# Kernel tuning notes

Hardware: AMD Instinct MI355X
Metric: run time of the kernel (lower is better)

The kernel has to match this reference:

```python
import jax, jax.numpy as jnp
import numpy as np

TEMPERATURE = 8.0  # sqrt(d_k), d_k = 64

def setup_inputs() -> dict:
    key = jax.random.key(0)
    k1, k2, k3, k4 = jax.random.split(key, 4)
    B, H, S, D = 2, 16, 2048, 64
    q = jax.random.normal(k1, (B, H, S, D), dtype=jnp.float32)
    k = jax.random.normal(k2, (B, H, S, D), dtype=jnp.float32)
    v = jax.random.normal(k3, (B, H, S, D), dtype=jnp.float32)
    # dwm: distance-weight matrix broadcast over heads
    dwm = jax.random.uniform(k4, (B, 1, S, S), dtype=jnp.float32)
    sigma = jnp.ones((1,), dtype=jnp.float32)
    return {"q": q, "k": k, "v": v, "dwm": dwm, "sigma": sigma}

def reference(q, k, v, dwm, sigma):
    # scores: [B,H,S,S]
    attn = jnp.einsum("bhsd,bhtd->bhst", q / TEMPERATURE, k)
    g = jnp.exp(dwm / (sigma ** 2))  # broadcasts [B,1,S,S] -> [B,H,S,S]
    attn = jnp.abs(attn * g)
    attn = jax.nn.softmax(attn, axis=-1)  # dropout is identity in eval
    output = jnp.einsum("bhst,bhtd->bhsd", attn, v)
    return (output, attn)
```

## Files before the change

### kernel.cpp

```cpp
#include <hip/hip_runtime.h>
#include <hip/hip_fp16.h>

#define NB 2
#define NH 16
#define NS 2048
#define ND 64
#define BM 64
#define BN 64
#define NT (NS / BN)
#define TILE_BYTES 24576
#define KV_BYTES ((size_t)NB * NH * NT * TILE_BYTES)

#define SW(r) ((((r) & 7) ^ (((r) & 8) >> 2)) << 4)

typedef _Float16 half8 __attribute__((ext_vector_type(8)));
typedef _Float16 half4 __attribute__((ext_vector_type(4)));
typedef float f32x4 __attribute__((ext_vector_type(4)));

#define GLDS16(gp, lp) __builtin_amdgcn_global_load_lds(                      \
    (const __attribute__((address_space(1))) void*)(gp),                      \
    (__attribute__((address_space(3))) void*)(lp), 16, 0, 0)

__global__ __launch_bounds__(256)
void prep_kv(const float* __restrict__ kg, const float* __restrict__ vg,
             char* __restrict__ ws)
{
    __shared__ _Float16 T[64][72];
    const int tile = blockIdx.x, bh = blockIdx.y, tid = threadIdx.x;
    const float* kp = kg + ((size_t)bh * NS + (size_t)tile * BN) * ND;
    const float* vp = vg + ((size_t)bh * NS + (size_t)tile * BN) * ND;
    char* img = ws + ((size_t)(bh * NT + tile)) * TILE_BYTES;

    #pragma unroll
    for (int i = 0; i < 2; ++i) {
        const int c = tid + i * 256;
        const int r = c >> 3, s = c & 7;
        const float* src = kp + r * ND + s * 8;
        float4 f0 = *(const float4*)src;
        float4 f1 = *(const float4*)(src + 4);
        float fv[8] = {f0.x, f0.y, f0.z, f0.w, f1.x, f1.y, f1.z, f1.w};
        half8 h, l;
        #pragma unroll
        for (int j = 0; j < 8; ++j) {
            _Float16 hh = (_Float16)fv[j];
            h[j] = hh; l[j] = (_Float16)(fv[j] - (float)hh);
        }
        const int off = r * 128 + ((s << 4) ^ SW(r));
        *(half8*)(img + off) = h;
        *(half8*)(img + 8192 + off) = l;
    }
    #pragma unroll
    for (int i = 0; i < 2; ++i) {
        const int c = tid + i * 256;
        const int t = c >> 3, ds = (c & 7) * 8;
        const float* src = vp + t * ND + ds;
        float4 f0 = *(const float4*)src;
        float4 f1 = *(const float4*)(src + 4);
        float fv[8] = {f0.x, f0.y, f0.z, f0.w, f1.x, f1.y, f1.z, f1.w};
        #pragma unroll
        for (int j = 0; j < 8; ++j) T[t][ds + j] = (_Float16)fv[j];
    }
    __syncthreads();
    #pragma unroll
    for (int i = 0; i < 2; ++i) {
        const int c = tid + i * 256;
        const int d = c >> 3, s = c & 7;
        half8 h;
        #pragma unroll
        for (int j = 0; j < 8; ++j) h[j] = T[s * 8 + j][d];
        *(half8*)(img + 16384 + d * 128 + ((s << 4) ^ SW(d))) = h;
    }
}

__global__ __launch_bounds__(256, 5)
void attn_fused(const float* __restrict__ qg, const char* __restrict__ kvws,
                const float* __restrict__ dwm, const float* __restrict__ sig,
                float* __restrict__ out0, float* __restrict__ attn)
{
    __shared__ char lds[32768];
    char* const Khi = lds;
    char* const Klo = lds + 8192;
    char* const Vs  = lds + 16384;
    char* const Ps  = lds + 24576;

    const int tid  = threadIdx.x;
    const int wave = tid >> 6;
    const int lane = tid & 63;
    const int quad = lane >> 4;
    const int lc   = lane & 15;

    const int mtile = blockIdx.x;
    const int bh    = blockIdx.y;
    const int b     = bh >> 4;

    const float sv = sig[0];
    const float inv_s2 = 1.0f / (sv * sv);

    const float* qp  = qg  + (size_t)bh * NS * ND + (size_t)mtile * BM * ND;
    const char*  kvb = kvws + (size_t)bh * NT * TILE_BYTES;
    const float* dp  = dwm + (size_t)b  * NS * NS + (size_t)mtile * BM * NS;
    float* op = out0 + (size_t)bh * NS * ND + (size_t)mtile * BM * ND;
    float* ap = attn + (size_t)bh * NS * NS + (size_t)mtile * BM * NS;

    half8 aqh0, aql0, aqh1, aql1;
    {
        const float* qr = qp + (size_t)(wave * 16 + lc) * ND + quad * 8;
        float4 f0 = *(const float4*)qr;
        float4 f1 = *(const float4*)(qr + 4);
        float4 f2 = *(const float4*)(qr + 32);
        float4 f3 = *(const float4*)(qr + 36);
        float v0[8] = {f0.x, f0.y, f0.z, f0.w, f1.x, f1.y, f1.z, f1.w};
        float v1[8] = {f2.x, f2.y, f2.z, f2.w, f3.x, f3.y, f3.z, f3.w};
        #pragma unroll
        for (int j = 0; j < 8; j++) {
            float x = v0[j] * 0.125f;
            _Float16 h = (_Float16)x;
            aqh0[j] = h; aql0[j] = (_Float16)(x - (float)h);
            x = v1[j] * 0.125f;
            h = (_Float16)x;
            aqh1[j] = h; aql1[j] = (_Float16)(x - (float)h);
        }
    }

    float lsum[4] = {0.f, 0.f, 0.f, 0.f};

    for (int t = 0; t < NT; ++t) {
        const char* img = kvb + (size_t)t * TILE_BYTES;
        __syncthreads();
        GLDS16(img +         tid * 16, Khi +        tid * 16);
        GLDS16(img +  4096 + tid * 16, Khi + 4096 + tid * 16);
        GLDS16(img +  8192 + tid * 16, Klo +        tid * 16);
        GLDS16(img + 12288 + tid * 16, Klo + 4096 + tid * 16);
        __syncthreads();
        #pragma unroll
        for (int n = 0; n < 4; ++n) {
            const int rowK = n * 16 + lc;
            const int sw = SW(rowK);
            const char* kb = Khi + rowK * 128;
            const char* lb = Klo + rowK * 128;
            const half8 kh0 = *(const half8*)(kb + ((quad * 16) ^ sw));
            const half8 kh1 = *(const half8*)(kb + ((64 + quad * 16) ^ sw));
            const half8 kl0 = *(const half8*)(lb + ((quad * 16) ^ sw));
            const half8 kl1 = *(const half8*)(lb + ((64 + quad * 16) ^ sw));
            f32x4 c = {0.f, 0.f, 0.f, 0.f};
            c = __builtin_amdgcn_mfma_f32_16x16x32_f16(aqh0, kh0, c, 0, 0, 0);
            c = __builtin_amdgcn_mfma_f32_16x16x32_f16(aqh1, kh1, c, 0, 0, 0);
            c = __builtin_amdgcn_mfma_f32_16x16x32_f16(aql0, kh0, c, 0, 0, 0);
            c = __builtin_amdgcn_mfma_f32_16x16x32_f16(aql1, kh1, c, 0, 0, 0);
            c = __builtin_amdgcn_mfma_f32_16x16x32_f16(aqh0, kl0, c, 0, 0, 0);
            c = __builtin_amdgcn_mfma_f32_16x16x32_f16(aqh1, kl1, c, 0, 0, 0);
            #pragma unroll
            for (int r2 = 0; r2 < 4; ++r2) {
                const int lrow = wave * 16 + quad * 4 + r2;
                const int col  = t * BN + n * 16 + lc;
                const float g = __expf(dp[(size_t)lrow * NS + col] * inv_s2);
                lsum[r2] += __expf(fabsf(c[r2]) * g);
            }
        }
    }

    #pragma unroll
    for (int r2 = 0; r2 < 4; ++r2) {
        float s = lsum[r2];
        s += __shfl_xor(s, 1, 64);
        s += __shfl_xor(s, 2, 64);
        s += __shfl_xor(s, 4, 64);
        s += __shfl_xor(s, 8, 64);
        lsum[r2] = 1.0f / s;
    }

    f32x4 o[4];
    #pragma unroll
    for (int i = 0; i < 4; i++) o[i] = (f32x4){0.f, 0.f, 0.f, 0.f};

    for (int t = 0; t < NT; ++t) {
        const char* img = kvb + (size_t)t * TILE_BYTES;
        __syncthreads();
        GLDS16(img +         tid * 16, Khi +        tid * 16);
        GLDS16(img +  4096 + tid * 16, Khi + 4096 + tid * 16);
        GLDS16(img +  8192 + tid * 16, Klo +        tid * 16);
        GLDS16(img + 12288 + tid * 16, Klo + 4096 + tid * 16);
        GLDS16(img + 16384 + tid * 16, Vs  +        tid * 16);
        GLDS16(img + 20480 + tid * 16, Vs  + 4096 + tid * 16);
        __syncthreads();
        #pragma unroll
        for (int n = 0; n < 4; ++n) {
            const int rowK = n * 16 + lc;
            const int sw = SW(rowK);
            const char* kb = Khi + rowK * 128;
            const char* lb = Klo + rowK * 128;
            const half8 kh0 = *(const half8*)(kb + ((quad * 16) ^ sw));
            const half8 kh1 = *(const half8*)(kb + ((64 + quad * 16) ^ sw));
            const half8 kl0 = *(const half8*)(lb + ((quad * 16) ^ sw));
            const half8 kl1 = *(const half8*)(lb + ((64 + quad * 16) ^ sw));
            f32x4 c = {0.f, 0.f, 0.f, 0.f};
            c = __builtin_amdgcn_mfma_f32_16x16x32_f16(aqh0, kh0, c, 0, 0, 0);
            c = __builtin_amdgcn_mfma_f32_16x16x32_f16(aqh1, kh1, c, 0, 0, 0);
            c = __builtin_amdgcn_mfma_f32_16x16x32_f16(aql0, kh0, c, 0, 0, 0);
            c = __builtin_amdgcn_mfma_f32_16x16x32_f16(aql1, kh1, c, 0, 0, 0);
            c = __builtin_amdgcn_mfma_f32_16x16x32_f16(aqh0, kl0, c, 0, 0, 0);
            c = __builtin_amdgcn_mfma_f32_16x16x32_f16(aqh1, kl1, c, 0, 0, 0);
            #pragma unroll
            for (int r2 = 0; r2 < 4; ++r2) {
                const int lrow = wave * 16 + quad * 4 + r2;
                const int col  = t * BN + n * 16 + lc;
                const float g = __expf(dp[(size_t)lrow * NS + col] * inv_s2);
                const float p = __expf(fabsf(c[r2]) * g) * lsum[r2];
                *(_Float16*)(Ps + lrow * 128 +
                             (((n * 16 + lc) * 2) ^ SW(lrow))) = (_Float16)p;
            }
        }
        const int rowP = wave * 16 + lc;
        const int swp = SW(rowP);
        const half8 pa0 = *(const half8*)(Ps + rowP * 128 + ((quad * 16) ^ swp));
        const half8 pa1 = *(const half8*)(Ps + rowP * 128 + ((64 + quad * 16) ^ swp));

        {
            const int cl = lane & 15, rh = lane >> 4;
            #pragma unroll
            for (int g2 = 0; g2 < 4; ++g2) {
                const int row = wave * 16 + g2 * 4 + rh;
                const half4 ph = *(const half4*)(Ps + row * 128 +
                                                 ((cl * 8) ^ SW(row)));
                f32x4 s = {(float)ph[0], (float)ph[1], (float)ph[2], (float)ph[3]};
                __builtin_nontemporal_store(
                    s, (f32x4*)(ap + (size_t)row * NS + t * BN + cl * 4));
            }
        }

        #pragma unroll
        for (int n2 = 0; n2 < 4; ++n2) {
            const int dv = n2 * 16 + lc;
            const int swv = SW(dv);
            const char* vb = Vs + dv * 128;
            const half8 bv0 = *(const half8*)(vb + ((quad * 16) ^ swv));
            const half8 bv1 = *(const half8*)(vb + ((64 + quad * 16) ^ swv));
            o[n2] = __builtin_amdgcn_mfma_f32_16x16x32_f16(pa0, bv0, o[n2], 0, 0, 0);
            o[n2] = __builtin_amdgcn_mfma_f32_16x16x32_f16(pa1, bv1, o[n2], 0, 0, 0);
        }
    }

    #pragma unroll
    for (int n2 = 0; n2 < 4; ++n2) {
        #pragma unroll
        for (int r2 = 0; r2 < 4; ++r2) {
            const int lrow = wave * 16 + quad * 4 + r2;
            __builtin_nontemporal_store(o[n2][r2],
                                        &op[(size_t)lrow * ND + n2 * 16 + lc]);
        }
    }
}

#define KP 72
#define VP 72
#define PP 72

__global__ __launch_bounds__(256, 4)
void attn_fused_legacy(const float* __restrict__ qg, const float* __restrict__ kgl,
                       const float* __restrict__ vgl, const float* __restrict__ dwm,
                       const float* __restrict__ sig, float* __restrict__ out0,
                       float* __restrict__ attn)
{
    __shared__ _Float16 Khi[BN * KP];
    __shared__ _Float16 Klo[BN * KP];
    __shared__ _Float16 Vsl[ND * VP];
    __shared__ _Float16 Psl[BM * PP];

    const int tid  = threadIdx.x;
    const int wave = tid >> 6;
    const int lane = tid & 63;
    const int quad = lane >> 4;
    const int lc   = lane & 15;

    const int mtile = blockIdx.x;
    const int bh    = blockIdx.y;
    const int b     = bh >> 4;

    const float sv = sig[0];
    const float inv_s2 = 1.0f / (sv * sv);

    const float* qp = qg  + (size_t)bh * NS * ND + (size_t)mtile * BM * ND;
    const float* kp = kgl + (size_t)bh * NS * ND;
    const float* vp = vgl + (size_t)bh * NS * ND;
    const float* dp = dwm + (size_t)b  * NS * NS + (size_t)mtile * BM * NS;
    float* op = out0 + (size_t)bh * NS * ND + (size_t)mtile * BM * ND;
    float* ap = attn + (size_t)bh * NS * NS + (size_t)mtile * BM * NS;

    half8 aqh0, aql0, aqh1, aql1;
    {
        const float* qr = qp + (size_t)(wave * 16 + lc) * ND + quad * 8;
        float4 f0 = *(const float4*)qr;
        float4 f1 = *(const float4*)(qr + 4);
        float4 f2 = *(const float4*)(qr + 32);
        float4 f3 = *(const float4*)(qr + 36);
        float v0[8] = {f0.x, f0.y, f0.z, f0.w, f1.x, f1.y, f1.z, f1.w};
        float v1[8] = {f2.x, f2.y, f2.z, f2.w, f3.x, f3.y, f3.z, f3.w};
        #pragma unroll
        for (int j = 0; j < 8; j++) {
            float x = v0[j] * 0.125f;
            _Float16 h = (_Float16)x;
            aqh0[j] = h; aql0[j] = (_Float16)(x - (float)h);
            x = v1[j] * 0.125f;
            h = (_Float16)x;
            aqh1[j] = h; aql1[j] = (_Float16)(x - (float)h);
        }
    }

    auto stageK = [&](int t0) {
        const int r  = tid >> 2;
        const int ds = (tid & 3) * 16;
        const float* s = kp + (size_t)(t0 + r) * ND + ds;
        float4 f0 = *(const float4*)s;
        float4 f1 = *(const float4*)(s + 4);
        float4 f2 = *(const float4*)(s + 8);
        float4 f3 = *(const float4*)(s + 12);
        float fv[16] = {f0.x, f0.y, f0.z, f0.w, f1.x, f1.y, f1.z, f1.w,
                        f2.x, f2.y, f2.z, f2.w, f3.x, f3.y, f3.z, f3.w};
        half8 h0, h1, l0, l1;
        #pragma unroll
        for (int i = 0; i < 8; i++) {
            _Float16 h = (_Float16)fv[i];
            h0[i] = h; l0[i] = (_Float16)(fv[i] - (float)h);
            h = (_Float16)fv[8 + i];
            h1[i] = h; l1[i] = (_Float16)(fv[8 + i] - (float)h);
        }
        *(half8*)&Khi[r * KP + ds]     = h0;
        *(half8*)&Khi[r * KP + ds + 8] = h1;
        *(half8*)&Klo[r * KP + ds]     = l0;
        *(half8*)&Klo[r * KP + ds + 8] = l1;
    };

    auto stageV = [&](int t0) {
        const int tp = tid >> 3;
        const int ds = (tid & 7) * 8;
        const float4* sa = (const float4*)(vp + (size_t)(t0 + 2 * tp) * ND + ds);
        const float4* sb = (const float4*)(vp + (size_t)(t0 + 2 * tp + 1) * ND + ds);
        float4 a0 = sa[0], a1 = sa[1];
        float4 b0 = sb[0], b1 = sb[1];
        float av[8] = {a0.x, a0.y, a0.z, a0.w, a1.x, a1.y, a1.z, a1.w};
        float bv[8] = {b0.x, b0.y, b0.z, b0.w, b1.x, b1.y, b1.z, b1.w};
        unsigned int* Vdw = (unsigned int*)Vsl;
        #pragma unroll
        for (int i = 0; i < 8; i++) {
            const int d  = ds + i;
            const int dw = d * (VP / 2) + (tp ^ (((d >> 3) & 7) << 2));
            union { _Float16 h[2]; unsigned int u; } pk;
            pk.h[0] = (_Float16)av[i];
            pk.h[1] = (_Float16)bv[i];
            Vdw[dw] = pk.u;
        }
    };

    float lsum[4] = {0.f, 0.f, 0.f, 0.f};

    for (int t0 = 0; t0 < NS; t0 += BN) {
        __syncthreads();
        stageK(t0);
        __syncthreads();
        #pragma unroll
        for (int n = 0; n < 4; n++) {
            const half8 kh0 = *(const half8*)&Khi[(n * 16 + lc) * KP + quad * 8];
            const half8 kh1 = *(const half8*)&Khi[(n * 16 + lc) * KP + quad * 8 + 32];
            const half8 kl0 = *(const half8*)&Klo[(n * 16 + lc) * KP + quad * 8];
            const half8 kl1 = *(const half8*)&Klo[(n * 16 + lc) * KP + quad * 8 + 32];
            f32x4 c = {0.f, 0.f, 0.f, 0.f};
            c = __builtin_amdgcn_mfma_f32_16x16x32_f16(aqh0, kh0, c, 0, 0, 0);
            c = __builtin_amdgcn_mfma_f32_16x16x32_f16(aqh1, kh1, c, 0, 0, 0);
            c = __builtin_amdgcn_mfma_f32_16x16x32_f16(aql0, kh0, c, 0, 0, 0);
            c = __builtin_amdgcn_mfma_f32_16x16x32_f16(aql1, kh1, c, 0, 0, 0);
            c = __builtin_amdgcn_mfma_f32_16x16x32_f16(aqh0, kl0, c, 0, 0, 0);
            c = __builtin_amdgcn_mfma_f32_16x16x32_f16(aqh1, kl1, c, 0, 0, 0);
            #pragma unroll
            for (int r2 = 0; r2 < 4; r2++) {
                const int lrow = wave * 16 + quad * 4 + r2;
                const int col  = t0 + n * 16 + lc;
                const float g = __expf(dp[(size_t)lrow * NS + col] * inv_s2);
                const float z = fabsf(c[r2] * g);
                lsum[r2] += __expf(z);
            }
        }
    }

    #pragma unroll
    for (int r2 = 0; r2 < 4; r2++) {
        float s = lsum[r2];
        s += __shfl_xor(s, 1, 64);
        s += __shfl_xor(s, 2, 64);
        s += __shfl_xor(s, 4, 64);
        s += __shfl_xor(s, 8, 64);
        lsum[r2] = 1.0f / s;
    }

    f32x4 o[4];
    #pragma unroll
    for (int i = 0; i < 4; i++) o[i] = (f32x4){0.f, 0.f, 0.f, 0.f};

    for (int t0 = 0; t0 < NS; t0 += BN) {
        __syncthreads();
        stageK(t0);
        stageV(t0);
        __syncthreads();
        #pragma unroll
        for (int n = 0; n < 4; n++) {
            const half8 kh0 = *(const half8*)&Khi[(n * 16 + lc) * KP + quad * 8];
            const half8 kh1 = *(const half8*)&Khi[(n * 16 + lc) * KP + quad * 8 + 32];
            const half8 kl0 = *(const half8*)&Klo[(n * 16 + lc) * KP + quad * 8];
            const half8 kl1 = *(const half8*)&Klo[(n * 16 + lc) * KP + quad * 8 + 32];
            f32x4 c = {0.f, 0.f, 0.f, 0.f};
            c = __builtin_amdgcn_mfma_f32_16x16x32_f16(aqh0, kh0, c, 0, 0, 0);
            c = __builtin_amdgcn_mfma_f32_16x16x32_f16(aqh1, kh1, c, 0, 0, 0);
            c = __builtin_amdgcn_mfma_f32_16x16x32_f16(aql0, kh0, c, 0, 0, 0);
            c = __builtin_amdgcn_mfma_f32_16x16x32_f16(aql1, kh1, c, 0, 0, 0);
            c = __builtin_amdgcn_mfma_f32_16x16x32_f16(aqh0, kl0, c, 0, 0, 0);
            c = __builtin_amdgcn_mfma_f32_16x16x32_f16(aqh1, kl1, c, 0, 0, 0);
            #pragma unroll
            for (int r2 = 0; r2 < 4; r2++) {
                const int lrow = wave * 16 + quad * 4 + r2;
                const int col  = t0 + n * 16 + lc;
                const float g = __expf(dp[(size_t)lrow * NS + col] * inv_s2);
                const float z = fabsf(c[r2] * g);
                const float p = __expf(z) * lsum[r2];
                Psl[(size_t)lrow * PP + n * 16 + lc] = (_Float16)p;
            }
        }
        const half8 pa0 = *(const half8*)&Psl[(wave * 16 + lc) * PP + quad * 8];
        const half8 pa1 = *(const half8*)&Psl[(wave * 16 + lc) * PP + quad * 8 + 32];

        {
            float* arow = ap + (size_t)(wave * 16 + lc) * NS + t0 + quad * 8;
            f32x4 s0 = {(float)pa0[0], (float)pa0[1], (float)pa0[2], (float)pa0[3]};
            f32x4 s1 = {(float)pa0[4], (float)pa0[5], (float)pa0[6], (float)pa0[7]};
            f32x4 s2 = {(float)pa1[0], (float)pa1[1], (float)pa1[2], (float)pa1[3]};
            f32x4 s3 = {(float)pa1[4], (float)pa1[5], (float)pa1[6], (float)pa1[7]};
            __builtin_nontemporal_store(s0, (f32x4*)arow);
            __builtin_nontemporal_store(s1, (f32x4*)(arow + 4));
            __builtin_nontemporal_store(s2, (f32x4*)(arow + 32));
            __builtin_nontemporal_store(s3, (f32x4*)(arow + 36));
        }

        #pragma unroll
        for (int n2 = 0; n2 < 4; n2++) {
            const int dv  = n2 * 16 + lc;
            const int fd  = ((dv >> 3) & 7) << 2;
            const int dwb = dv * (VP / 2);
            const half8 bv0 = *(const half8*)((const char*)Vsl +
                               (size_t)((dwb + ((quad * 4) ^ fd)) * 4));
            const half8 bv1 = *(const half8*)((const char*)Vsl +
                               (size_t)((dwb + ((16 + quad * 4) ^ fd)) * 4));
            o[n2] = __builtin_amdgcn_mfma_f32_16x16x32_f16(pa0, bv0, o[n2], 0, 0, 0);
            o[n2] = __builtin_amdgcn_mfma_f32_16x16x32_f16(pa1, bv1, o[n2], 0, 0, 0);
        }
    }

    #pragma unroll
    for (int n2 = 0; n2 < 4; n2++) {
        #pragma unroll
        for (int r2 = 0; r2 < 4; r2++) {
            const int lrow = wave * 16 + quad * 4 + r2;
            __builtin_nontemporal_store(o[n2][r2],
                                        &op[(size_t)lrow * ND + n2 * 16 + lc]);
        }
    }
}

extern "C" void kernel_launch(void* const* d_in, const int* in_sizes, int n_in,
                              void* d_out, int out_size, void* d_ws, size_t ws_size,
                              hipStream_t stream) {
    (void)in_sizes; (void)n_in; (void)out_size;
    const float* q   = (const float*)d_in[0];
    const float* k   = (const float*)d_in[1];
    const float* v   = (const float*)d_in[2];
    const float* dwm = (const float*)d_in[3];
    const float* sig = (const float*)d_in[4];
    float* out0 = (float*)d_out;
    float* attn = out0 + (size_t)NB * NH * NS * ND;

    if (d_ws != nullptr && ws_size >= KV_BYTES) {
        char* ws = (char*)d_ws;
        prep_kv<<<dim3(NT, NB * NH), dim3(256), 0, stream>>>(k, v, ws);
        attn_fused<<<dim3(NS / BM, NB * NH), dim3(256), 0, stream>>>(
            q, ws, dwm, sig, out0, attn);
    } else {
        dim3 grid(NS / BM, NB * NH);
        attn_fused_legacy<<<grid, dim3(256), 0, stream>>>(
            q, k, v, dwm, sig, out0, attn);
    }
}
```

Baseline: 864.9 us.

## Double-buffer K tiles in LDS to overlap global loads with compute

Adds a second K hi/lo tile buffer in shared memory and prefetches the next tile with global_load_lds while the current tile is used, in both the row-sum pass and the output pass. Explicit vmcnt waits and barriers replace the paired __syncthreads around each load. The goal is to hide load latency behind MFMA and exp work. In exchange LDS grows from 32 KB to 48 KB and launch bounds drop from 5 to 3 blocks per CU, so occupancy falls. The second pass relies on vmcnt(4) ordering to wait for V while the prefetch stays in flight, which is delicate.

```diff
diff --git a/kernel.cpp b/kernel.cpp
--- a/kernel.cpp
+++ b/kernel.cpp
@@ -72,16 +72,14 @@
     }
 }
 
-__global__ __launch_bounds__(256, 5)
+__global__ __launch_bounds__(256, 3)
 void attn_fused(const float* __restrict__ qg, const char* __restrict__ kvws,
                 const float* __restrict__ dwm, const float* __restrict__ sig,
                 float* __restrict__ out0, float* __restrict__ attn)
 {
-    __shared__ char lds[32768];
-    char* const Khi = lds;
-    char* const Klo = lds + 8192;
-    char* const Vs  = lds + 16384;
-    char* const Ps  = lds + 24576;
+    __shared__ char lds[49152];
+    char* const Vs = lds + 32768;
+    char* const Ps = lds + 40960;
 
     const int tid  = threadIdx.x;
     const int wave = tid >> 6;
@@ -124,24 +122,33 @@
 
     float lsum[4] = {0.f, 0.f, 0.f, 0.f};
 
+    {
+        #pragma unroll
+        for (int j = 0; j < 4; ++j)
+            GLDS16(kvb + j * 4096 + tid * 16, lds + j * 4096 + tid * 16);
+        asm volatile("s_waitcnt vmcnt(0)" ::: "memory");
+        __builtin_amdgcn_s_barrier();
+    }
+
     for (int t = 0; t < NT; ++t) {
-        const char* img = kvb + (size_t)t * TILE_BYTES;
-        __syncthreads();
-        GLDS16(img +         tid * 16, Khi +        tid * 16);
-        GLDS16(img +  4096 + tid * 16, Khi + 4096 + tid * 16);
-        GLDS16(img +  8192 + tid * 16, Klo +        tid * 16);
-        GLDS16(img + 12288 + tid * 16, Klo + 4096 + tid * 16);
-        __syncthreads();
+        char* const kb = lds + ((t & 1) << 14);
+        if (t + 1 < NT) {
+            const char* nimg = kvb + (size_t)(t + 1) * TILE_BYTES;
+            char* nb = lds + (((t + 1) & 1) << 14);
+            #pragma unroll
+            for (int j = 0; j < 4; ++j)
+                GLDS16(nimg + j * 4096 + tid * 16, nb + j * 4096 + tid * 16);
+        }
         #pragma unroll
         for (int n = 0; n < 4; ++n) {
             const int rowK = n * 16 + lc;
             const int sw = SW(rowK);
-            const char* kb = Khi + rowK * 128;
-            const char* lb = Klo + rowK * 128;
-            const half8 kh0 = *(const half8*)(kb + ((quad * 16) ^ sw));
-            const half8 kh1 = *(const half8*)(kb + ((64 + quad * 16) ^ sw));
-            const half8 kl0 = *(const half8*)(lb + ((quad * 16) ^ sw));
-            const half8 kl1 = *(const half8*)(lb + ((64 + quad * 16) ^ sw));
+            const char* kkb = kb + rowK * 128;
+            const char* llb = kb + 8192 + rowK * 128;
+            const half8 kh0 = *(const half8*)(kkb + ((quad * 16) ^ sw));
+            const half8 kh1 = *(const half8*)(kkb + ((64 + quad * 16) ^ sw));
+            const half8 kl0 = *(const half8*)(llb + ((quad * 16) ^ sw));
+            const half8 kl1 = *(const half8*)(llb + ((64 + quad * 16) ^ sw));
             f32x4 c = {0.f, 0.f, 0.f, 0.f};
             c = __builtin_amdgcn_mfma_f32_16x16x32_f16(aqh0, kh0, c, 0, 0, 0);
             c = __builtin_amdgcn_mfma_f32_16x16x32_f16(aqh1, kh1, c, 0, 0, 0);
@@ -157,6 +164,8 @@
                 lsum[r2] += __expf(fabsf(c[r2]) * g);
             }
         }
+        asm volatile("s_waitcnt vmcnt(0)" ::: "memory");
+        __builtin_amdgcn_s_barrier();
     }
 
     #pragma unroll
@@ -173,26 +182,38 @@
     #pragma unroll
     for (int i = 0; i < 4; i++) o[i] = (f32x4){0.f, 0.f, 0.f, 0.f};
 
+    {
+        #pragma unroll
+        for (int j = 0; j < 4; ++j)
+            GLDS16(kvb + j * 4096 + tid * 16, lds + j * 4096 + tid * 16);
+        asm volatile("s_waitcnt vmcnt(0)" ::: "memory");
+        __builtin_amdgcn_s_barrier();
+    }
+
     for (int t = 0; t < NT; ++t) {
         const char* img = kvb + (size_t)t * TILE_BYTES;
-        __syncthreads();
-        GLDS16(img +         tid * 16, Khi +        tid * 16);
-        GLDS16(img +  4096 + tid * 16, Khi + 4096 + tid * 16);
-        GLDS16(img +  8192 + tid * 16, Klo +        tid * 16);
-        GLDS16(img + 12288 + tid * 16, Klo + 4096 + tid * 16);
-        GLDS16(img + 16384 + tid * 16, Vs  +        tid * 16);
-        GLDS16(img + 20480 + tid * 16, Vs  + 4096 + tid * 16);
-        __syncthreads();
+        char* const kb = lds + ((t & 1) << 14);
+
+        GLDS16(img + 16384 +        tid * 16, Vs +        tid * 16);
+        GLDS16(img + 16384 + 4096 + tid * 16, Vs + 4096 + tid * 16);
+        if (t + 1 < NT) {
+            const char* nimg = kvb + (size_t)(t + 1) * TILE_BYTES;
+            char* nb = lds + (((t + 1) & 1) << 14);
+            #pragma unroll
+            for (int j = 0; j < 4; ++j)
+                GLDS16(nimg + j * 4096 + tid * 16, nb + j * 4096 + tid * 16);
+        }
+
         #pragma unroll
         for (int n = 0; n < 4; ++n) {
             const int rowK = n * 16 + lc;
             const int sw = SW(rowK);
-            const char* kb = Khi + rowK * 128;
-            const char* lb = Klo + rowK * 128;
-            const half8 kh0 = *(const half8*)(kb + ((quad * 16) ^ sw));
-            const half8 kh1 = *(const half8*)(kb + ((64 + quad * 16) ^ sw));
-            const half8 kl0 = *(const half8*)(lb + ((quad * 16) ^ sw));
-            const half8 kl1 = *(const half8*)(lb + ((64 + quad * 16) ^ sw));
+            const char* kkb = kb + rowK * 128;
+            const char* llb = kb + 8192 + rowK * 128;
+            const half8 kh0 = *(const half8*)(kkb + ((quad * 16) ^ sw));
+            const half8 kh1 = *(const half8*)(kkb + ((64 + quad * 16) ^ sw));
+            const half8 kl0 = *(const half8*)(llb + ((quad * 16) ^ sw));
+            const half8 kl1 = *(const half8*)(llb + ((64 + quad * 16) ^ sw));
             f32x4 c = {0.f, 0.f, 0.f, 0.f};
             c = __builtin_amdgcn_mfma_f32_16x16x32_f16(aqh0, kh0, c, 0, 0, 0);
             c = __builtin_amdgcn_mfma_f32_16x16x32_f16(aqh1, kh1, c, 0, 0, 0);
@@ -210,6 +231,11 @@
                              (((n * 16 + lc) * 2) ^ SW(lrow))) = (_Float16)p;
             }
         }
+
+        if (t + 1 < NT) { asm volatile("s_waitcnt vmcnt(4)" ::: "memory"); }
+        else            { asm volatile("s_waitcnt vmcnt(0)" ::: "memory"); }
+        __builtin_amdgcn_s_barrier();
+
         const int rowP = wave * 16 + lc;
         const int swp = SW(rowP);
         const half8 pa0 = *(const half8*)(Ps + rowP * 128 + ((quad * 16) ^ swp));
@@ -238,6 +264,9 @@
             o[n2] = __builtin_amdgcn_mfma_f32_16x16x32_f16(pa0, bv0, o[n2], 0, 0, 0);
             o[n2] = __builtin_amdgcn_mfma_f32_16x16x32_f16(pa1, bv1, o[n2], 0, 0, 0);
         }
+
+        asm volatile("s_waitcnt vmcnt(0)" ::: "memory");
+        __builtin_amdgcn_s_barrier();
     }
 
     #pragma unroll
```

New measurement: 850.9 us. Within noise of the previous version (-1.6%).
